# Kernel tuning notes

Hardware: AMD Instinct MI355X
Metric: run time of the kernel (lower is better)

The kernel has to match this reference:

```python
import jax, jax.numpy as jnp
import numpy as np

BS, NQ, D = 4, 12500, 256
HEADS, LEVELS, POINTS = 8, 2, 4
HD = D // HEADS
D_FF = 2048
SHAPES = ((100, 100), (50, 50))   # (H, W) per level; sum(H*W) == NQ
STARTS = (0, 10000)


def layer_norm(x, g, b, eps=1e-5):
    m = x.mean(-1, keepdims=True)
    v = ((x - m) ** 2).mean(-1, keepdims=True)
    return (x - m) * jax.lax.rsqrt(v + eps) * g + b


def bilinear_sample(value_l, loc, H, W):
    # value_l: (bs, heads, H*W, hd); loc: (bs, heads, nq, P, 2) normalized [0,1]
    # matches F.grid_sample(align_corners=False, padding_mode='zeros')
    x = loc[..., 0] * W - 0.5
    y = loc[..., 1] * H - 0.5
    x0 = jnp.floor(x)
    y0 = jnp.floor(y)
    wx1 = x - x0
    wy1 = y - y0
    wx0 = 1.0 - wx1
    wy0 = 1.0 - wy1
    x0i = x0.astype(jnp.int32)
    y0i = y0.astype(jnp.int32)

    def gather(xi, yi):
        valid = (xi >= 0) & (xi < W) & (yi >= 0) & (yi < H)
        idx = jnp.clip(yi, 0, H - 1) * W + jnp.clip(xi, 0, W - 1)  # (bs,heads,nq,P)
        b, h, nq, P = idx.shape
        g = jnp.take_along_axis(value_l, idx.reshape(b, h, nq * P, 1), axis=2)
        g = g.reshape(b, h, nq, P, -1)
        return g * valid[..., None].astype(g.dtype)

    g00 = gather(x0i, y0i)
    g10 = gather(x0i + 1, y0i)
    g01 = gather(x0i, y0i + 1)
    g11 = gather(x0i + 1, y0i + 1)
    return (g00 * (wx0 * wy0)[..., None] + g10 * (wx1 * wy0)[..., None]
            + g01 * (wx0 * wy1)[..., None] + g11 * (wx1 * wy1)[..., None])


def setup_inputs() -> dict:
    key = jax.random.key(0)
    ks = jax.random.split(key, 20)
    s = 0.02
    inp = {
        'query': jax.random.normal(ks[0], (BS, NQ, D), jnp.float32),
        'reference_points': jax.random.uniform(ks[1], (BS, NQ, LEVELS, 2), jnp.float32),
        'w_off': s * jax.random.normal(ks[2], (D, HEADS * LEVELS * POINTS * 2), jnp.float32),
        'b_off': s * jax.random.normal(ks[3], (HEADS * LEVELS * POINTS * 2,), jnp.float32),
        'w_attn': s * jax.random.normal(ks[4], (D, HEADS * LEVELS * POINTS), jnp.float32),
        'b_attn': s * jax.random.normal(ks[5], (HEADS * LEVELS * POINTS,), jnp.float32),
        'w_val': s * jax.random.normal(ks[6], (D, D), jnp.float32),
        'b_val': jnp.zeros((D,), jnp.float32),
        'w_out': s * jax.random.normal(ks[7], (D, D), jnp.float32),
        'b_out': jnp.zeros((D,), jnp.float32),
        'w1': s * jax.random.normal(ks[8], (D, D_FF), jnp.float32),
        'b1': jnp.zeros((D_FF,), jnp.float32),
        'w2': s * jax.random.normal(ks[9], (D_FF, D), jnp.float32),
        'b2': jnp.zeros((D,), jnp.float32),
        'ln0_g': jnp.ones((D,), jnp.float32),
        'ln0_b': jnp.zeros((D,), jnp.float32),
        'ln1_g': jnp.ones((D,), jnp.float32),
        'ln1_b': jnp.zeros((D,), jnp.float32),
    }
    return inp


def reference(query, reference_points, w_off, b_off, w_attn, b_attn, w_val, b_val,
              w_out, b_out, w1, b1, w2, b2, ln0_g, ln0_b, ln1_g, ln1_b):
    bs, nq, _ = query.shape
    # value projection; encoder self-attention: value == query tokens
    value = (query @ w_val + b_val).reshape(bs, nq, HEADS, HD).transpose(0, 2, 1, 3)  # (bs,heads,nv,hd)
    off = (query @ w_off + b_off).reshape(bs, nq, HEADS, LEVELS, POINTS, 2)
    aw = (query @ w_attn + b_attn).reshape(bs, nq, HEADS, LEVELS * POINTS)
    aw = jax.nn.softmax(aw, axis=-1).reshape(bs, nq, HEADS, LEVELS, POINTS)

    out = jnp.zeros((bs, HEADS, nq, HD), query.dtype)
    for l, (H, W) in enumerate(SHAPES):
        normalizer = jnp.array([W, H], query.dtype)
        # (bs,nq,heads,P,2)
        loc = reference_points[:, :, None, l, None, :] + off[:, :, :, l] / normalizer
        loc = loc.transpose(0, 2, 1, 3, 4)  # (bs,heads,nq,P,2)
        v_l = value[:, :, STARTS[l]:STARTS[l] + H * W]  # (bs,heads,H*W,hd)
        sampled = bilinear_sample(v_l, loc, H, W)       # (bs,heads,nq,P,hd)
        w_l = aw[:, :, :, l].transpose(0, 2, 1, 3)      # (bs,heads,nq,P)
        out = out + (sampled * w_l[..., None]).sum(axis=3)

    attn_out = out.transpose(0, 2, 1, 3).reshape(bs, nq, D) @ w_out + b_out
    x = layer_norm(query + attn_out, ln0_g, ln0_b)
    h = jax.nn.relu(x @ w1 + b1)
    x = layer_norm(x + (h @ w2 + b2), ln1_g, ln1_b)
    return x
```

## Files before the change

### kernel.cpp

```cpp
#include <hip/hip_runtime.h>


#define NQv 12500
#define BSv 4
#define Dv  256
#define DFF 2048

typedef __attribute__((ext_vector_type(8))) __bf16 bf16x8;
typedef __attribute__((ext_vector_type(4))) float f32x4;

__device__ __forceinline__ ushort f32_to_bf16(float f) {
  unsigned u = __float_as_uint(f);
  u += 0x7FFFu + ((u >> 16) & 1u);
  return (ushort)(u >> 16);
}
__device__ __forceinline__ float bf16_to_f32(ushort u) {
  return __uint_as_float(((unsigned)u) << 16);
}

__global__ __launch_bounds__(256) void conv_bf16_kernel(
    const float* __restrict__ in, ushort* __restrict__ out, int n4) {
  int i = blockIdx.x * 256 + threadIdx.x;
  if (i >= n4) return;
  float4 v = reinterpret_cast<const float4*>(in)[i];
  uint2 st;
  st.x = (unsigned)f32_to_bf16(v.x) | ((unsigned)f32_to_bf16(v.y) << 16);
  st.y = (unsigned)f32_to_bf16(v.z) | ((unsigned)f32_to_bf16(v.w) << 16);
  reinterpret_cast<uint2*>(out)[i] = st;
}

__global__ __launch_bounds__(256) void ttrans_kernel(
    const float* __restrict__ in, ushort* __restrict__ out, int K, int N) {
  __shared__ ushort tl[64][65];
  const int n0 = blockIdx.x * 64, k0 = blockIdx.y * 64;
  const int t = threadIdx.x;
#pragma unroll
  for (int i = 0; i < 16; ++i) {
    int idx = t + 256 * i;
    int r = idx >> 6, c = idx & 63;
    tl[r][c] = f32_to_bf16(in[(size_t)(k0 + r) * N + n0 + c]);
  }
  __syncthreads();
#pragma unroll
  for (int i = 0; i < 16; ++i) {
    int idx = t + 256 * i;
    int r = idx >> 6, c = idx & 63;
    out[(size_t)(n0 + r) * K + k0 + c] = tl[c][r];
  }
}

__global__ __launch_bounds__(256) void build_wcat_kernel(
    const float* __restrict__ w_val, const float* __restrict__ w_off,
    const float* __restrict__ w_attn, const float* __restrict__ b_val,
    const float* __restrict__ b_off, const float* __restrict__ b_attn,
    ushort* __restrict__ wcat, float* __restrict__ bcat) {
  int i = blockIdx.x * 256 + threadIdx.x;
  if (i < 448 * 256) {
    int n = i >> 8, k = i & 255;
    float v = (n < 256) ? w_val[(size_t)k * 256 + n]
              : (n < 384) ? w_off[(size_t)k * 128 + (n - 256)]
                          : w_attn[(size_t)k * 64 + (n - 384)];
    wcat[i] = f32_to_bf16(v);
  }
  if (i < 512)
    bcat[i] = (i < 256) ? b_val[i] : (i < 384) ? b_off[i - 256]
              : (i < 448) ? b_attn[i - 384] : 0.f;
}

#define TBM 128
#define TBN 128
#define TBK 32

template <int RELU, int NMASK>
__global__ __launch_bounds__(256) void gemm128_kernel(
    const ushort* __restrict__ A, const ushort* __restrict__ Bt,
    const float* __restrict__ bias, ushort* __restrict__ C,
    int M, int K, int ldc, int Nreal) {
  __shared__ ushort lds[4][TBM * TBK];

  const int t = threadIdx.x;
  const int wid = t >> 6, lane = t & 63;
  const int wr = wid >> 1, wc = wid & 1;
  const int m0 = blockIdx.y * TBM;
  const int n0 = blockIdx.x * TBN;

  int srowA[2], srowB[2], gsl[2];
#pragma unroll
  for (int i = 0; i < 2; i++) {
    int row = i * 64 + (t >> 2);
    int ar = m0 + row;
    srowA[i] = (ar < M) ? ar : (M - 1);
    srowB[i] = n0 + row;
    gsl[i] = ((t & 3) ^ ((row >> 1) & 3)) * 8;
  }

  f32x4 acc[4][4] = {};
  const int nt = K / TBK;
  int cur = 0;

#pragma unroll
  for (int i = 0; i < 2; i++) {
    const int ldsoff = (i * 256 + wid * 64) * 8;
    __builtin_amdgcn_global_load_lds(
        (const __attribute__((address_space(1))) void*)(A + (size_t)srowA[i] * K + gsl[i]),
        (__attribute__((address_space(3))) void*)(lds[0] + ldsoff), 16, 0, 0);
    __builtin_amdgcn_global_load_lds(
        (const __attribute__((address_space(1))) void*)(Bt + (size_t)srowB[i] * K + gsl[i]),
        (__attribute__((address_space(3))) void*)(lds[1] + ldsoff), 16, 0, 0);
  }
  __syncthreads();

  const int rl = lane & 15, kh = lane >> 4;
  for (int tk = 0; tk < nt; ++tk) {
    if (tk + 1 < nt) {
      const int k0 = (tk + 1) * TBK;
      const int nb = (cur ^ 1) * 2;
#pragma unroll
      for (int i = 0; i < 2; i++) {
        const int ldsoff = (i * 256 + wid * 64) * 8;
        __builtin_amdgcn_global_load_lds(
            (const __attribute__((address_space(1))) void*)(A + (size_t)srowA[i] * K + k0 + gsl[i]),
            (__attribute__((address_space(3))) void*)(lds[nb] + ldsoff), 16, 0, 0);
        __builtin_amdgcn_global_load_lds(
            (const __attribute__((address_space(1))) void*)(Bt + (size_t)srowB[i] * K + k0 + gsl[i]),
            (__attribute__((address_space(3))) void*)(lds[nb + 1] + ldsoff), 16, 0, 0);
      }
    }
    {
      const ushort* As = lds[cur * 2];
      const ushort* Bs = lds[cur * 2 + 1];
      bf16x8 afr[4], bfr[4];
#pragma unroll
      for (int ni = 0; ni < 4; ni++) {
        int rowb = wc * 64 + ni * 16 + rl;
        int p = kh ^ ((rowb >> 1) & 3);
        bfr[ni] = *reinterpret_cast<const bf16x8*>(Bs + rowb * 32 + p * 8);
      }
#pragma unroll
      for (int mi = 0; mi < 4; mi++) {
        int rowa = wr * 64 + mi * 16 + rl;
        int p = kh ^ ((rowa >> 1) & 3);
        afr[mi] = *reinterpret_cast<const bf16x8*>(As + rowa * 32 + p * 8);
      }
#pragma unroll
      for (int mi = 0; mi < 4; mi++)
#pragma unroll
        for (int ni = 0; ni < 4; ni++)
          acc[mi][ni] = __builtin_amdgcn_mfma_f32_16x16x32_bf16(afr[mi], bfr[ni], acc[mi][ni], 0, 0, 0);
    }
    __syncthreads();
    cur ^= 1;
  }

  ushort* ldsC = lds[0];
  const int rgrp = lane >> 4, cl = lane & 15;
#pragma unroll
  for (int pass = 0; pass < 2; ++pass) {
    if (wr == pass) {
#pragma unroll
      for (int mi = 0; mi < 4; mi++) {
#pragma unroll
        for (int ni = 0; ni < 4; ni++) {
          int col = wc * 64 + ni * 16 + cl;
          float bv = bias[n0 + col];
#pragma unroll
          for (int r = 0; r < 4; r++) {
            int rloc = mi * 16 + rgrp * 4 + r;
            float v = acc[mi][ni][r] + bv;
            if (RELU) v = fmaxf(v, 0.f);
            ldsC[rloc * 132 + col] = f32_to_bf16(v);
          }
        }
      }
    }
    __syncthreads();
    {
      int rloc = t >> 2;
      int row = m0 + pass * 64 + rloc;
      if (row < M) {
#pragma unroll
        for (int j = 0; j < 4; j++) {
          int col = (t & 3) * 32 + j * 8;
          if (!NMASK || n0 + col < Nreal) {
            uint4 v = *reinterpret_cast<const uint4*>(ldsC + rloc * 132 + col);
            *reinterpret_cast<uint4*>(C + (size_t)row * ldc + n0 + col) = v;
          }
        }
      }
    }
    __syncthreads();
  }
}

__global__ __launch_bounds__(512, 1) void ffn_ln_fused_kernel(
    const ushort* __restrict__ xb,
    const ushort* __restrict__ w1t,
    const float* __restrict__ b1,
    const ushort* __restrict__ w2t,
    const float* __restrict__ b2,
    const float* __restrict__ g1, const float* __restrict__ be1,
    float* __restrict__ out,
    int M) {
  __shared__ ushort lds_all[74752];
  ushort* As = lds_all;
  ushort* Hs = lds_all + 32768;
  ushort* stg0 = lds_all + 50176;

  const int t = threadIdx.x;
  const int wv = t >> 6;
  const int wm = wv >> 2;
  const int wn = wv & 3;
  const int lane = t & 63;
  const int rl = lane & 15, kq = lane >> 4;
  const int cl = lane & 15, g4 = lane >> 4;
  const int m0 = blockIdx.x * 128;

  const int b1row = t >> 3, b1slot = t & 7;
  const int b2row = t >> 2, b2slot = t & 3;

  auto stg = [&](int i) { return stg0 + i * 8192; };

  auto issueB1 = [&](int p, int j, ushort* dst) {
#pragma unroll
    for (int ii = 0; ii < 2; ++ii) {
      int row = b1row + 64 * ii;
      int g = b1slot ^ (row & 7);
      __builtin_amdgcn_global_load_lds(
          (const __attribute__((address_space(1))) void*)(
              w1t + (size_t)(p * 128 + row) * 256 + j * 64 + g * 8),
          (__attribute__((address_space(3))) void*)(dst + (t + 512 * ii) * 8), 16, 0, 0);
    }
  };
  auto issueB2 = [&](int p, int tt, ushort* dst) {
#pragma unroll
    for (int ii = 0; ii < 2; ++ii) {
      int row = b2row + 128 * ii;
      int g = b2slot ^ ((row >> 1) & 3);
      __builtin_amdgcn_global_load_lds(
          (const __attribute__((address_space(1))) void*)(
              w2t + (size_t)row * 2048 + p * 128 + tt * 32 + g * 8),
          (__attribute__((address_space(3))) void*)(dst + (t + 512 * ii) * 8), 16, 0, 0);
    }
  };

#pragma unroll
  for (int ii = 0; ii < 8; ++ii) {
    int row = (t >> 5) + 16 * ii;
    int g = (t & 31) ^ (row & 7);
    int ar = m0 + row; ar = (ar < M) ? ar : (M - 1);
    __builtin_amdgcn_global_load_lds(
        (const __attribute__((address_space(1))) void*)(xb + (size_t)ar * 256 + g * 8),
        (__attribute__((address_space(3))) void*)(As + (t + 512 * ii) * 8), 16, 0, 0);
  }
  issueB1(0, 0, stg(0));
  issueB1(0, 1, stg(1));

  f32x4 acc1[4][2] = {};
  f32x4 accF[4][4] = {};
  int cur = 0;

  for (int p = 0; p < 16; ++p) {
#pragma unroll
    for (int j = 0; j < 8; ++j) {
      int tgt = cur + 2; if (tgt >= 3) tgt -= 3;
      if (j <= 5) {
        const int j2 = j + 2;
        const int p2 = p + (j2 >> 3);
        if ((j2 & 7) < 4) issueB1(p2, j2 & 3, stg(tgt));
        else issueB2(p2, (j2 & 7) - 4, stg(tgt));
        asm volatile("s_waitcnt vmcnt(4) lgkmcnt(0)" ::: "memory");
      } else if (p < 15) {
        const int j2m = (j + 2) & 7;
        issueB1(p + 1, j2m, stg(tgt));
        asm volatile("s_waitcnt vmcnt(4) lgkmcnt(0)" ::: "memory");
      } else if (j == 6) {
        asm volatile("s_waitcnt vmcnt(2) lgkmcnt(0)" ::: "memory");
      } else {
        asm volatile("s_waitcnt vmcnt(0) lgkmcnt(0)" ::: "memory");
      }
      __builtin_amdgcn_s_barrier();
      __builtin_amdgcn_sched_barrier(0);

      const ushort* Bs = stg(cur);
      if (j < 4) {
        __builtin_amdgcn_s_setprio(1);
#pragma unroll
        for (int kk = 0; kk < 2; ++kk) {
          bf16x8 afr[4], bfr[2];
          const int slotA = j * 8 + kk * 4 + kq;
#pragma unroll
          for (int mi = 0; mi < 4; mi++) {
            int rowa = wm * 64 + mi * 16 + rl;
            afr[mi] = *reinterpret_cast<const bf16x8*>(As + rowa * 256 + (slotA ^ (rowa & 7)) * 8);
          }
          const int slotB = kk * 4 + kq;
#pragma unroll
          for (int ni = 0; ni < 2; ni++) {
            int rowb = wn * 32 + ni * 16 + rl;
            bfr[ni] = *reinterpret_cast<const bf16x8*>(Bs + rowb * 64 + (slotB ^ (rowb & 7)) * 8);
          }
#pragma unroll
          for (int mi = 0; mi < 4; mi++)
#pragma unroll
            for (int ni = 0; ni < 2; ni++)
              acc1[mi][ni] = __builtin_amdgcn_mfma_f32_16x16x32_bf16(afr[mi], bfr[ni], acc1[mi][ni], 0, 0, 0);
        }
        __builtin_amdgcn_s_setprio(0);
        if (j == 3) {
#pragma unroll
          for (int ni = 0; ni < 2; ni++) {
            int col = wn * 32 + ni * 16 + cl;
            float b1v = b1[p * 128 + col];
#pragma unroll
            for (int mi = 0; mi < 4; mi++) {
#pragma unroll
              for (int r = 0; r < 4; r++) {
                int row = wm * 64 + mi * 16 + g4 * 4 + r;
                Hs[row * 136 + col] = f32_to_bf16(fmaxf(acc1[mi][ni][r] + b1v, 0.f));
              }
            }
          }
#pragma unroll
          for (int mi = 0; mi < 4; mi++)
#pragma unroll
            for (int ni = 0; ni < 2; ni++)
              acc1[mi][ni] = (f32x4){0.f, 0.f, 0.f, 0.f};
        }
      } else {
        const int tt = j - 4;
        bf16x8 afr[4], bfr[4];
#pragma unroll
        for (int mi = 0; mi < 4; mi++) {
          int rowa = wm * 64 + mi * 16 + rl;
          afr[mi] = *reinterpret_cast<const bf16x8*>(Hs + rowa * 136 + (tt * 4 + kq) * 8);
        }
#pragma unroll
        for (int ni = 0; ni < 4; ni++) {
          int rowb = wn * 64 + ni * 16 + rl;
          bfr[ni] = *reinterpret_cast<const bf16x8*>(Bs + rowb * 32 + (kq ^ ((rowb >> 1) & 3)) * 8);
        }
        __builtin_amdgcn_s_setprio(1);
#pragma unroll
        for (int mi = 0; mi < 4; mi++)
#pragma unroll
          for (int ni = 0; ni < 4; ni++)
            accF[mi][ni] = __builtin_amdgcn_mfma_f32_16x16x32_bf16(afr[mi], bfr[ni], accF[mi][ni], 0, 0, 0);
        __builtin_amdgcn_s_setprio(0);
      }
      cur = cur + 1; if (cur >= 3) cur -= 3;
    }
  }

  float* ptab = (float*)stg0;
  float* mtab = (float*)(stg0 + 2048);

  float b2c[4], g1c[4], bec[4];
#pragma unroll
  for (int ni = 0; ni < 4; ni++) {
    int col = wn * 64 + ni * 16 + cl;
    b2c[ni] = b2[col]; g1c[ni] = g1[col]; bec[ni] = be1[col];
  }
#pragma unroll
  for (int mi = 0; mi < 4; mi++) {
#pragma unroll
    for (int ni = 0; ni < 4; ni++) {
      int col = wn * 64 + ni * 16 + cl;
#pragma unroll
      for (int r = 0; r < 4; r++) {
        int row = wm * 64 + mi * 16 + g4 * 4 + r;
        ushort xv = As[row * 256 + ((col >> 3) ^ (row & 7)) * 8 + (col & 7)];
        accF[mi][ni][r] += b2c[ni] + bf16_to_f32(xv);
      }
    }
  }
#pragma unroll
  for (int mi = 0; mi < 4; mi++) {
#pragma unroll
    for (int r = 0; r < 4; r++) {
      float s = accF[mi][0][r] + accF[mi][1][r] + accF[mi][2][r] + accF[mi][3][r];
      float sq = accF[mi][0][r] * accF[mi][0][r] + accF[mi][1][r] * accF[mi][1][r] +
                 accF[mi][2][r] * accF[mi][2][r] + accF[mi][3][r] * accF[mi][3][r];
#pragma unroll
      for (int o = 1; o < 16; o <<= 1) {
        s += __shfl_xor(s, o, 64);
        sq += __shfl_xor(sq, o, 64);
      }
      if (cl == 0) {
        int row = wm * 64 + mi * 16 + g4 * 4 + r;
        ptab[(row * 4 + wn) * 2 + 0] = s;
        ptab[(row * 4 + wn) * 2 + 1] = sq;
      }
    }
  }
  __syncthreads();
  {
    int row = t >> 2, part = t & 3;
    float s = ptab[(row * 4 + part) * 2 + 0];
    float sq = ptab[(row * 4 + part) * 2 + 1];
    s += __shfl_xor(s, 1, 64);  sq += __shfl_xor(sq, 1, 64);
    s += __shfl_xor(s, 2, 64);  sq += __shfl_xor(sq, 2, 64);
    if (part == 0) {
      float mean = s * (1.f / 256.f);
      float var = sq * (1.f / 256.f) - mean * mean;
      mtab[row * 2 + 0] = mean;
      mtab[row * 2 + 1] = rsqrtf(var + 1e-5f);
    }
  }
  __syncthreads();
#pragma unroll
  for (int mi = 0; mi < 4; mi++) {
#pragma unroll
    for (int r = 0; r < 4; r++) {
      int row = wm * 64 + mi * 16 + g4 * 4 + r;
      float2 ms = *reinterpret_cast<const float2*>(mtab + row * 2);
      int grow = m0 + row;
      if (grow < M) {
#pragma unroll
        for (int ni = 0; ni < 4; ni++) {
          int col = wn * 64 + ni * 16 + cl;
          out[(size_t)grow * 256 + col] = (accF[mi][ni][r] - ms.x) * ms.y * g1c[ni] + bec[ni];
        }
      }
    }
  }
}

__global__ __launch_bounds__(256) void deform_attn_kernel(
    const ushort* __restrict__ pcat, const float* __restrict__ refp,
    ushort* __restrict__ out, int total) {
  int tid = blockIdx.x * 256 + threadIdx.x;
  if (tid >= total) return;
  int c0 = (tid & 3) * 8;
  int idx = tid >> 2;
  int h = idx & 7;
  int row = idx >> 3;
  int bl = row / NQv;

  const ushort* prow = pcat + (size_t)row * 448;

  ushort awr[8];
  *reinterpret_cast<uint4*>(awr) = *reinterpret_cast<const uint4*>(prow + 384 + h * 8);
  float lg[8], mx = -1e30f;
#pragma unroll
  for (int i = 0; i < 8; i++) { lg[i] = bf16_to_f32(awr[i]); mx = fmaxf(mx, lg[i]); }
  float ssum = 0.f;
#pragma unroll
  for (int i = 0; i < 8; i++) { lg[i] = __expf(lg[i] - mx); ssum += lg[i]; }
  float inv = 1.f / ssum;

  ushort ofr[16];
  *reinterpret_cast<uint4*>(ofr)     = *reinterpret_cast<const uint4*>(prow + 256 + h * 16);
  *reinterpret_cast<uint4*>(ofr + 8) = *reinterpret_cast<const uint4*>(prow + 256 + h * 16 + 8);
  float4 rp = *reinterpret_cast<const float4*>(refp + (size_t)row * 4);

  float acc8[8] = {};
  const int Ws[2] = {100, 50}, Hs2[2] = {100, 50}, Ss[2] = {0, 10000};
#pragma unroll
  for (int l = 0; l < 2; l++) {
    const int W = Ws[l], H = Hs2[l];
    float fx = (l ? rp.z : rp.x) * (float)W - 0.5f;
    float fy = (l ? rp.w : rp.y) * (float)H - 0.5f;
    const ushort* vbase = pcat + ((size_t)bl * NQv + Ss[l]) * 448 + h * 32 + c0;
#pragma unroll
    for (int p = 0; p < 4; p++) {
      float x = fx + bf16_to_f32(ofr[l * 8 + p * 2 + 0]);
      float y = fy + bf16_to_f32(ofr[l * 8 + p * 2 + 1]);
      float x0f = floorf(x), y0f = floorf(y);
      float wx1 = x - x0f, wy1 = y - y0f;
      float wx0 = 1.f - wx1, wy0 = 1.f - wy1;
      int x0 = (int)x0f, y0 = (int)y0f;
      float aw = lg[l * 4 + p] * inv;

      float cw[4] = {aw * wx0 * wy0, aw * wx1 * wy0, aw * wx0 * wy1, aw * wx1 * wy1};
      int cx[4] = {x0, x0 + 1, x0, x0 + 1};
      int cy[4] = {y0, y0, y0 + 1, y0 + 1};
#pragma unroll
      for (int c = 0; c < 4; c++) {
        int xi = cx[c], yi = cy[c];
        if (xi >= 0 && xi < W && yi >= 0 && yi < H) {
          ushort vr[8];
          *reinterpret_cast<uint4*>(vr) =
              *reinterpret_cast<const uint4*>(vbase + (size_t)(yi * W + xi) * 448);
          float w = cw[c];
#pragma unroll
          for (int j = 0; j < 8; j++) acc8[j] += w * bf16_to_f32(vr[j]);
        }
      }
    }
  }

  ushort st[8];
#pragma unroll
  for (int j = 0; j < 8; j++) st[j] = f32_to_bf16(acc8[j]);
  *reinterpret_cast<uint4*>(out + (size_t)row * 256 + h * 32 + c0) =
      *reinterpret_cast<uint4*>(st);
}

__global__ __launch_bounds__(256) void ln0_kernel(
    const float* __restrict__ A, const ushort* __restrict__ B,
    const float* __restrict__ gamma, const float* __restrict__ beta,
    ushort* __restrict__ outb, int M) {
  int row = blockIdx.x * 4 + (threadIdx.x >> 6);
  int lane = threadIdx.x & 63;
  if (row >= M) return;
  size_t base = (size_t)row * 256 + lane * 4;
  float4 a = *reinterpret_cast<const float4*>(A + base);
  uint2 braw = *reinterpret_cast<const uint2*>(B + base);
  float x0 = a.x + bf16_to_f32((ushort)(braw.x & 0xffffu));
  float x1 = a.y + bf16_to_f32((ushort)(braw.x >> 16));
  float x2 = a.z + bf16_to_f32((ushort)(braw.y & 0xffffu));
  float x3 = a.w + bf16_to_f32((ushort)(braw.y >> 16));
  float s = x0 + x1 + x2 + x3;
  float sq = x0 * x0 + x1 * x1 + x2 * x2 + x3 * x3;
#pragma unroll
  for (int o = 1; o < 64; o <<= 1) {
    s += __shfl_xor(s, o, 64);
    sq += __shfl_xor(sq, o, 64);
  }
  float mean = s * (1.f / 256.f);
  float var = sq * (1.f / 256.f) - mean * mean;
  float rs = rsqrtf(var + 1e-5f);
  float4 gv = *reinterpret_cast<const float4*>(gamma + lane * 4);
  float4 bv = *reinterpret_cast<const float4*>(beta + lane * 4);
  float o0 = (x0 - mean) * rs * gv.x + bv.x;
  float o1 = (x1 - mean) * rs * gv.y + bv.y;
  float o2 = (x2 - mean) * rs * gv.z + bv.z;
  float o3 = (x3 - mean) * rs * gv.w + bv.w;
  uint2 st;
  st.x = (unsigned)f32_to_bf16(o0) | ((unsigned)f32_to_bf16(o1) << 16);
  st.y = (unsigned)f32_to_bf16(o2) | ((unsigned)f32_to_bf16(o3) << 16);
  *reinterpret_cast<uint2*>(outb + base) = st;
}

extern "C" void kernel_launch(void* const* d_in, const int* in_sizes, int n_in,
                              void* d_out, int out_size, void* d_ws, size_t ws_size,
                              hipStream_t stream) {
  const float* query  = (const float*)d_in[0];
  const float* refp   = (const float*)d_in[1];
  const float* w_off  = (const float*)d_in[2];
  const float* b_off  = (const float*)d_in[3];
  const float* w_attn = (const float*)d_in[4];
  const float* b_attn = (const float*)d_in[5];
  const float* w_val  = (const float*)d_in[6];
  const float* b_val  = (const float*)d_in[7];
  const float* w_out  = (const float*)d_in[8];
  const float* b_out  = (const float*)d_in[9];
  const float* w1     = (const float*)d_in[10];
  const float* b1     = (const float*)d_in[11];
  const float* w2     = (const float*)d_in[12];
  const float* b2     = (const float*)d_in[13];
  const float* ln0g   = (const float*)d_in[14];
  const float* ln0b   = (const float*)d_in[15];
  const float* ln1g   = (const float*)d_in[16];
  const float* ln1b   = (const float*)d_in[17];
  float* outp = (float*)d_out;

  char* ws = (char*)d_ws;
  size_t woff = 0;
  auto walloc = [&](size_t bytes) { size_t r = woff; woff += (bytes + 255) & ~(size_t)255; return r; };
  ushort* wcat = (ushort*)(ws + walloc((size_t)512 * 256 * 2));
  float*  bcat = (float*)(ws + walloc(512 * 4));
  ushort* wqt  = (ushort*)(ws + walloc((size_t)256 * 256 * 2));
  ushort* w1t  = (ushort*)(ws + walloc((size_t)DFF * 256 * 2));
  ushort* w2t  = (ushort*)(ws + walloc((size_t)256 * DFF * 2));
  char* arena = ws + woff;
  size_t arena_sz = (ws_size > woff) ? (ws_size - woff) : 0;

  int nb = ((size_t)BSv * NQv * 1920 + (1u << 20) <= arena_sz) ? BSv : 1;
  const int R = nb * NQv;
  ushort* qb   = (ushort*)arena;
  ushort* pcat = (ushort*)(arena + (size_t)R * 512);
  ushort* samp = (ushort*)(arena + (size_t)R * 1408);
  ushort* proj = qb;
  ushort* xb   = samp;

  build_wcat_kernel<<<dim3(448), dim3(256), 0, stream>>>(
      w_val, w_off, w_attn, b_val, b_off, b_attn, wcat, bcat);
  ttrans_kernel<<<dim3(4, 4), dim3(256), 0, stream>>>(w_out, wqt, Dv, Dv);
  ttrans_kernel<<<dim3(DFF / 64, 4), dim3(256), 0, stream>>>(w1, w1t, Dv, DFF);
  ttrans_kernel<<<dim3(4, DFF / 64), dim3(256), 0, stream>>>(w2, w2t, DFF, Dv);

  const int MT = (R + TBM - 1) / TBM;

  for (int c = 0; c < BSv / nb; c++) {
    const int row0 = c * R;
    const float* qrow = query + (size_t)row0 * Dv;

    conv_bf16_kernel<<<dim3((R * 64 + 255) / 256), dim3(256), 0, stream>>>(qrow, qb, R * 64);

    gemm128_kernel<0, 1><<<dim3(4, MT), dim3(256), 0, stream>>>(
        qb, wcat, bcat, pcat, R, Dv, 448, 448);

    deform_attn_kernel<<<dim3((R * 32 + 255) / 256), dim3(256), 0, stream>>>(
        pcat, refp + (size_t)row0 * 4, samp, R * 32);

    gemm128_kernel<0, 0><<<dim3(2, MT), dim3(256), 0, stream>>>(
        samp, wqt, b_out, proj, R, Dv, 256, 256);

    ln0_kernel<<<dim3((R + 3) / 4), dim3(256), 0, stream>>>(qrow, proj, ln0g, ln0b, xb, R);

    ffn_ln_fused_kernel<<<dim3((R + 127) / 128), dim3(512), 0, stream>>>(
        xb, w1t, b1, w2t, b2, ln1g, ln1b, outp + (size_t)row0 * 256, R);
  }
}
```

Before: 338.4 us.

## Restructure FFN pipeline to load LDS fragments before barrier and overlap MFMA

Reorders the fused FFN main loop so each step issues the next global-to-LDS prefetch first, then reads the A/B fragments into registers, and only then barriers and runs the MFMAs. The wait on outstanding loads moves to the end of the step, and a second barrier is added there. The aim is to overlap LDS fragment reads and global prefetch with MFMA work and to relax the vmcnt waits. In exchange each step now has two barriers and holds more fragment registers at once. The ordering between the stage-buffer writes and reads is subtle, so a synchronisation mistake could give wrong results.

Measured after the change: 357.8 us. +5.8%, slower.

```diff
diff --git a/kernel.cpp b/kernel.cpp
--- a/kernel.cpp
+++ b/kernel.cpp
@@ -254,6 +254,8 @@
   }
   issueB1(0, 0, stg(0));
   issueB1(0, 1, stg(1));
+  asm volatile("s_waitcnt vmcnt(2)" ::: "memory");
+  __builtin_amdgcn_s_barrier();
 
   f32x4 acc1[4][2] = {};
   f32x4 accF[4][4] = {};
@@ -263,90 +265,97 @@
 #pragma unroll
     for (int j = 0; j < 8; ++j) {
       int tgt = cur + 2; if (tgt >= 3) tgt -= 3;
-      if (j <= 5) {
-        const int j2 = j + 2;
-        const int p2 = p + (j2 >> 3);
-        if ((j2 & 7) < 4) issueB1(p2, j2 & 3, stg(tgt));
-        else issueB2(p2, (j2 & 7) - 4, stg(tgt));
-        asm volatile("s_waitcnt vmcnt(4) lgkmcnt(0)" ::: "memory");
-      } else if (p < 15) {
-        const int j2m = (j + 2) & 7;
-        issueB1(p + 1, j2m, stg(tgt));
-        asm volatile("s_waitcnt vmcnt(4) lgkmcnt(0)" ::: "memory");
-      } else if (j == 6) {
-        asm volatile("s_waitcnt vmcnt(2) lgkmcnt(0)" ::: "memory");
-      } else {
-        asm volatile("s_waitcnt vmcnt(0) lgkmcnt(0)" ::: "memory");
-      }
-      __builtin_amdgcn_s_barrier();
-      __builtin_amdgcn_sched_barrier(0);
+      if (!(p == 15 && j >= 6)) {
+        const int j2 = (j + 2) & 7;
+        const int p2 = p + ((j + 2) >> 3);
+        if (j2 < 4) issueB1(p2, j2, stg(tgt));
+        else issueB2(p2, j2 - 4, stg(tgt));
+      }
 
       const ushort* Bs = stg(cur);
+      bf16x8 a1[4][2], b1f[2][2];
+      bf16x8 a2[4], b2f[4];
       if (j < 4) {
-        __builtin_amdgcn_s_setprio(1);
 #pragma unroll
         for (int kk = 0; kk < 2; ++kk) {
-          bf16x8 afr[4], bfr[2];
           const int slotA = j * 8 + kk * 4 + kq;
 #pragma unroll
           for (int mi = 0; mi < 4; mi++) {
             int rowa = wm * 64 + mi * 16 + rl;
-            afr[mi] = *reinterpret_cast<const bf16x8*>(As + rowa * 256 + (slotA ^ (rowa & 7)) * 8);
+            a1[mi][kk] = *reinterpret_cast<const bf16x8*>(As + rowa * 256 + (slotA ^ (rowa & 7)) * 8);
           }
           const int slotB = kk * 4 + kq;
 #pragma unroll
           for (int ni = 0; ni < 2; ni++) {
             int rowb = wn * 32 + ni * 16 + rl;
-            bfr[ni] = *reinterpret_cast<const bf16x8*>(Bs + rowb * 64 + (slotB ^ (rowb & 7)) * 8);
+            b1f[ni][kk] = *reinterpret_cast<const bf16x8*>(Bs + rowb * 64 + (slotB ^ (rowb & 7)) * 8);
           }
+        }
+      } else {
+        const int tt = j - 4;
+#pragma unroll
+        for (int mi = 0; mi < 4; mi++) {
+          int rowa = wm * 64 + mi * 16 + rl;
+          a2[mi] = *reinterpret_cast<const bf16x8*>(Hs + rowa * 136 + (tt * 4 + kq) * 8);
+        }
+#pragma unroll
+        for (int ni = 0; ni < 4; ni++) {
+          int rowb = wn * 64 + ni * 16 + rl;
+          b2f[ni] = *reinterpret_cast<const bf16x8*>(Bs + rowb * 32 + (kq ^ ((rowb >> 1) & 3)) * 8);
+        }
+      }
+
+      __builtin_amdgcn_s_barrier();
+      asm volatile("s_waitcnt lgkmcnt(0)" ::: "memory");
+      __builtin_amdgcn_sched_barrier(0);
+
+      __builtin_amdgcn_s_setprio(1);
+      if (j < 4) {
+#pragma unroll
+        for (int kk = 0; kk < 2; ++kk)
 #pragma unroll
           for (int mi = 0; mi < 4; mi++)
 #pragma unroll
             for (int ni = 0; ni < 2; ni++)
-              acc1[mi][ni] = __builtin_amdgcn_mfma_f32_16x16x32_bf16(afr[mi], bfr[ni], acc1[mi][ni], 0, 0, 0);
-        }
-        __builtin_amdgcn_s_setprio(0);
-        if (j == 3) {
-#pragma unroll
-          for (int ni = 0; ni < 2; ni++) {
-            int col = wn * 32 + ni * 16 + cl;
-            float b1v = b1[p * 128 + col];
-#pragma unroll
-            for (int mi = 0; mi < 4; mi++) {
-#pragma unroll
-              for (int r = 0; r < 4; r++) {
-                int row = wm * 64 + mi * 16 + g4 * 4 + r;
-                Hs[row * 136 + col] = f32_to_bf16(fmaxf(acc1[mi][ni][r] + b1v, 0.f));
-              }
+              acc1[mi][ni] = __builtin_amdgcn_mfma_f32_16x16x32_bf16(a1[mi][kk], b1f[ni][kk], acc1[mi][ni], 0, 0, 0);
+      } else {
+#pragma unroll
+        for (int mi = 0; mi < 4; mi++)
+#pragma unroll
+          for (int ni = 0; ni < 4; ni++)
+            accF[mi][ni] = __builtin_amdgcn_mfma_f32_16x16x32_bf16(a2[mi], b2f[ni], accF[mi][ni], 0, 0, 0);
+      }
+      __builtin_amdgcn_s_setprio(0);
+
+      if (j == 3) {
+#pragma unroll
+        for (int ni = 0; ni < 2; ni++) {
+          int col = wn * 32 + ni * 16 + cl;
+          float b1v = b1[p * 128 + col];
+#pragma unroll
+          for (int mi = 0; mi < 4; mi++) {
+#pragma unroll
+            for (int r = 0; r < 4; r++) {
+              int row = wm * 64 + mi * 16 + g4 * 4 + r;
+              Hs[row * 136 + col] = f32_to_bf16(fmaxf(acc1[mi][ni][r] + b1v, 0.f));
             }
           }
-#pragma unroll
-          for (int mi = 0; mi < 4; mi++)
-#pragma unroll
-            for (int ni = 0; ni < 2; ni++)
-              acc1[mi][ni] = (f32x4){0.f, 0.f, 0.f, 0.f};
-        }
+        }
+#pragma unroll
+        for (int mi = 0; mi < 4; mi++)
+#pragma unroll
+          for (int ni = 0; ni < 2; ni++)
+            acc1[mi][ni] = (f32x4){0.f, 0.f, 0.f, 0.f};
+      }
+
+      if (!(p == 15 && j >= 6)) {
+        asm volatile("s_waitcnt vmcnt(2) lgkmcnt(0)" ::: "memory");
+      } else if (j == 6) {
+        asm volatile("s_waitcnt vmcnt(0) lgkmcnt(0)" ::: "memory");
       } else {
-        const int tt = j - 4;
-        bf16x8 afr[4], bfr[4];
-#pragma unroll
-        for (int mi = 0; mi < 4; mi++) {
-          int rowa = wm * 64 + mi * 16 + rl;
-          afr[mi] = *reinterpret_cast<const bf16x8*>(Hs + rowa * 136 + (tt * 4 + kq) * 8);
-        }
-#pragma unroll
-        for (int ni = 0; ni < 4; ni++) {
-          int rowb = wn * 64 + ni * 16 + rl;
-          bfr[ni] = *reinterpret_cast<const bf16x8*>(Bs + rowb * 32 + (kq ^ ((rowb >> 1) & 3)) * 8);
-        }
-        __builtin_amdgcn_s_setprio(1);
-#pragma unroll
-        for (int mi = 0; mi < 4; mi++)
-#pragma unroll
-          for (int ni = 0; ni < 4; ni++)
-            accF[mi][ni] = __builtin_amdgcn_mfma_f32_16x16x32_bf16(afr[mi], bfr[ni], accF[mi][ni], 0, 0, 0);
-        __builtin_amdgcn_s_setprio(0);
-      }
+        asm volatile("s_waitcnt lgkmcnt(0)" ::: "memory");
+      }
+      __builtin_amdgcn_s_barrier();
       cur = cur + 1; if (cur >= 3) cur -= 3;
     }
   }
```

## Fuse output projection GEMM with residual add and LayerNorm0

Applied to the files above, without the earlier changes.

Replaces the separate out-projection GEMM and ln0 kernel with one kernel. It computes a 64x256 tile with MFMA, double-buffers the B tiles, adds bias and the fp32 query residual, and applies LayerNorm in-register before writing bf16. This removes the bf16 proj intermediate round trip and one launch, and keeps the pre-LN sum in fp32. It also adds an initial wait and barrier to the FFN kernel before its main loop. The cost is a narrower M tile and strided scalar query loads in the epilogue.

After: 328.9 us. 1.03x faster.

```diff
diff --git a/kernel.cpp b/kernel.cpp
--- a/kernel.cpp
+++ b/kernel.cpp
@@ -189,6 +189,156 @@
       }
     }
     __syncthreads();
+  }
+}
+
+__global__ __launch_bounds__(256, 2) void outproj_ln0_kernel(
+    const ushort* __restrict__ samp,
+    const ushort* __restrict__ wqt,
+    const float* __restrict__ bias,
+    const float* __restrict__ query,
+    const float* __restrict__ g0, const float* __restrict__ be0,
+    ushort* __restrict__ xb,
+    int M) {
+  __shared__ ushort lds_all[32768];
+  ushort* As = lds_all;
+  ushort* ring0 = lds_all + 16384;
+
+  const int t = threadIdx.x;
+  const int wv = t >> 6;
+  const int lane = t & 63;
+  const int rl = lane & 15, kq = lane >> 4;
+  const int cl = lane & 15, g4 = lane >> 4;
+  const int m0 = blockIdx.x * 64;
+
+  ushort* ring[2] = {ring0, ring0 + 8192};
+
+  auto issueB = [&](int j, ushort* dst) {
+#pragma unroll
+    for (int ii = 0; ii < 4; ++ii) {
+      int row = (t >> 2) + 64 * ii;
+      int g = (t & 3) ^ ((row >> 1) & 3);
+      __builtin_amdgcn_global_load_lds(
+          (const __attribute__((address_space(1))) void*)(
+              wqt + (size_t)row * 256 + j * 32 + g * 8),
+          (__attribute__((address_space(3))) void*)(dst + ((size_t)t + 256 * ii) * 8), 16, 0, 0);
+    }
+  };
+
+#pragma unroll
+  for (int ii = 0; ii < 8; ++ii) {
+    int row = (t >> 5) + 8 * ii;
+    int g = (t & 31) ^ (row & 7);
+    int ar = m0 + row; ar = (ar < M) ? ar : (M - 1);
+    __builtin_amdgcn_global_load_lds(
+        (const __attribute__((address_space(1))) void*)(samp + (size_t)ar * 256 + g * 8),
+        (__attribute__((address_space(3))) void*)(As + ((size_t)t + 256 * ii) * 8), 16, 0, 0);
+  }
+  issueB(0, ring[0]);
+  __syncthreads();
+
+  f32x4 accF[4][4] = {};
+  int cur = 0;
+
+#pragma unroll
+  for (int j = 0; j < 8; ++j) {
+    if (j + 1 < 8) issueB(j + 1, ring[cur ^ 1]);
+    const ushort* Bs = ring[cur];
+    bf16x8 afr[4], bfr[4];
+    const int slotA = j * 4 + kq;
+#pragma unroll
+    for (int mi = 0; mi < 4; mi++) {
+      int rowa = mi * 16 + rl;
+      afr[mi] = *reinterpret_cast<const bf16x8*>(As + rowa * 256 + (slotA ^ (rowa & 7)) * 8);
+    }
+#pragma unroll
+    for (int ni = 0; ni < 4; ni++) {
+      int rowb = wv * 64 + ni * 16 + rl;
+      bfr[ni] = *reinterpret_cast<const bf16x8*>(Bs + rowb * 32 + (kq ^ ((rowb >> 1) & 3)) * 8);
+    }
+    __builtin_amdgcn_s_setprio(1);
+#pragma unroll
+    for (int mi = 0; mi < 4; mi++)
+#pragma unroll
+      for (int ni = 0; ni < 4; ni++)
+        accF[mi][ni] = __builtin_amdgcn_mfma_f32_16x16x32_bf16(afr[mi], bfr[ni], accF[mi][ni], 0, 0, 0);
+    __builtin_amdgcn_s_setprio(0);
+    __syncthreads();
+    cur ^= 1;
+  }
+
+  float* ptab = (float*)ring0;
+  float* mtab = (float*)(ring0 + 2048);
+
+  float bc[4], gc[4], bec[4];
+#pragma unroll
+  for (int ni = 0; ni < 4; ni++) {
+    int col = wv * 64 + ni * 16 + cl;
+    bc[ni] = bias[col]; gc[ni] = g0[col]; bec[ni] = be0[col];
+  }
+#pragma unroll
+  for (int mi = 0; mi < 4; mi++) {
+#pragma unroll
+    for (int ni = 0; ni < 4; ni++) {
+      int col = wv * 64 + ni * 16 + cl;
+#pragma unroll
+      for (int r = 0; r < 4; r++) {
+        int row = mi * 16 + g4 * 4 + r;
+        int qrow = m0 + row; qrow = (qrow < M) ? qrow : (M - 1);
+        accF[mi][ni][r] += bc[ni] + query[(size_t)qrow * 256 + col];
+      }
+    }
+  }
+#pragma unroll
+  for (int mi = 0; mi < 4; mi++) {
+#pragma unroll
+    for (int r = 0; r < 4; r++) {
+      float s = accF[mi][0][r] + accF[mi][1][r] + accF[mi][2][r] + accF[mi][3][r];
+      float sq = accF[mi][0][r] * accF[mi][0][r] + accF[mi][1][r] * accF[mi][1][r] +
+                 accF[mi][2][r] * accF[mi][2][r] + accF[mi][3][r] * accF[mi][3][r];
+#pragma unroll
+      for (int o = 1; o < 16; o <<= 1) {
+        s += __shfl_xor(s, o, 64);
+        sq += __shfl_xor(sq, o, 64);
+      }
+      if (cl == 0) {
+        int row = mi * 16 + g4 * 4 + r;
+        ptab[(row * 4 + wv) * 2 + 0] = s;
+        ptab[(row * 4 + wv) * 2 + 1] = sq;
+      }
+    }
+  }
+  __syncthreads();
+  {
+    int row = t >> 2, part = t & 3;
+    float s = ptab[(row * 4 + part) * 2 + 0];
+    float sq = ptab[(row * 4 + part) * 2 + 1];
+    s += __shfl_xor(s, 1, 64);  sq += __shfl_xor(sq, 1, 64);
+    s += __shfl_xor(s, 2, 64);  sq += __shfl_xor(sq, 2, 64);
+    if (part == 0) {
+      float mean = s * (1.f / 256.f);
+      float var = sq * (1.f / 256.f) - mean * mean;
+      mtab[row * 2 + 0] = mean;
+      mtab[row * 2 + 1] = rsqrtf(var + 1e-5f);
+    }
+  }
+  __syncthreads();
+#pragma unroll
+  for (int mi = 0; mi < 4; mi++) {
+#pragma unroll
+    for (int r = 0; r < 4; r++) {
+      int row = mi * 16 + g4 * 4 + r;
+      float2 ms = *reinterpret_cast<const float2*>(mtab + row * 2);
+      int grow = m0 + row;
+      if (grow < M) {
+#pragma unroll
+        for (int ni = 0; ni < 4; ni++) {
+          int col = wv * 64 + ni * 16 + cl;
+          xb[(size_t)grow * 256 + col] =
+              f32_to_bf16((accF[mi][ni][r] - ms.x) * ms.y * gc[ni] + bec[ni]);
+        }
+      }
+    }
   }
 }
 
@@ -254,6 +404,8 @@
   }
   issueB1(0, 0, stg(0));
   issueB1(0, 1, stg(1));
+  asm volatile("s_waitcnt vmcnt(2)" ::: "memory");
+  __builtin_amdgcn_s_barrier();
 
   f32x4 acc1[4][2] = {};
   f32x4 accF[4][4] = {};
@@ -328,23 +480,23 @@
         }
       } else {
         const int tt = j - 4;
-        bf16x8 afr[4], bfr[4];
+        bf16x8 a2f[4], b2f[4];
 #pragma unroll
         for (int mi = 0; mi < 4; mi++) {
           int rowa = wm * 64 + mi * 16 + rl;
-          afr[mi] = *reinterpret_cast<const bf16x8*>(Hs + rowa * 136 + (tt * 4 + kq) * 8);
+          a2f[mi] = *reinterpret_cast<const bf16x8*>(Hs + rowa * 136 + (tt * 4 + kq) * 8);
         }
 #pragma unroll
         for (int ni = 0; ni < 4; ni++) {
           int rowb = wn * 64 + ni * 16 + rl;
-          bfr[ni] = *reinterpret_cast<const bf16x8*>(Bs + rowb * 32 + (kq ^ ((rowb >> 1) & 3)) * 8);
+          b2f[ni] = *reinterpret_cast<const bf16x8*>(Bs + rowb * 32 + (kq ^ ((rowb >> 1) & 3)) * 8);
         }
         __builtin_amdgcn_s_setprio(1);
 #pragma unroll
         for (int mi = 0; mi < 4; mi++)
 #pragma unroll
           for (int ni = 0; ni < 4; ni++)
-            accF[mi][ni] = __builtin_amdgcn_mfma_f32_16x16x32_bf16(afr[mi], bfr[ni], accF[mi][ni], 0, 0, 0);
+            accF[mi][ni] = __builtin_amdgcn_mfma_f32_16x16x32_bf16(a2f[mi], b2f[ni], accF[mi][ni], 0, 0, 0);
         __builtin_amdgcn_s_setprio(0);
       }
       cur = cur + 1; if (cur >= 3) cur -= 3;
@@ -494,42 +646,6 @@
   for (int j = 0; j < 8; j++) st[j] = f32_to_bf16(acc8[j]);
   *reinterpret_cast<uint4*>(out + (size_t)row * 256 + h * 32 + c0) =
       *reinterpret_cast<uint4*>(st);
-}
-
-__global__ __launch_bounds__(256) void ln0_kernel(
-    const float* __restrict__ A, const ushort* __restrict__ B,
-    const float* __restrict__ gamma, const float* __restrict__ beta,
-    ushort* __restrict__ outb, int M) {
-  int row = blockIdx.x * 4 + (threadIdx.x >> 6);
-  int lane = threadIdx.x & 63;
-  if (row >= M) return;
-  size_t base = (size_t)row * 256 + lane * 4;
-  float4 a = *reinterpret_cast<const float4*>(A + base);
-  uint2 braw = *reinterpret_cast<const uint2*>(B + base);
-  float x0 = a.x + bf16_to_f32((ushort)(braw.x & 0xffffu));
-  float x1 = a.y + bf16_to_f32((ushort)(braw.x >> 16));
-  float x2 = a.z + bf16_to_f32((ushort)(braw.y & 0xffffu));
-  float x3 = a.w + bf16_to_f32((ushort)(braw.y >> 16));
-  float s = x0 + x1 + x2 + x3;
-  float sq = x0 * x0 + x1 * x1 + x2 * x2 + x3 * x3;
-#pragma unroll
-  for (int o = 1; o < 64; o <<= 1) {
-    s += __shfl_xor(s, o, 64);
-    sq += __shfl_xor(sq, o, 64);
-  }
-  float mean = s * (1.f / 256.f);
-  float var = sq * (1.f / 256.f) - mean * mean;
-  float rs = rsqrtf(var + 1e-5f);
-  float4 gv = *reinterpret_cast<const float4*>(gamma + lane * 4);
-  float4 bv = *reinterpret_cast<const float4*>(beta + lane * 4);
-  float o0 = (x0 - mean) * rs * gv.x + bv.x;
-  float o1 = (x1 - mean) * rs * gv.y + bv.y;
-  float o2 = (x2 - mean) * rs * gv.z + bv.z;
-  float o3 = (x3 - mean) * rs * gv.w + bv.w;
-  uint2 st;
-  st.x = (unsigned)f32_to_bf16(o0) | ((unsigned)f32_to_bf16(o1) << 16);
-  st.y = (unsigned)f32_to_bf16(o2) | ((unsigned)f32_to_bf16(o3) << 16);
-  *reinterpret_cast<uint2*>(outb + base) = st;
 }
 
 extern "C" void kernel_launch(void* const* d_in, const int* in_sizes, int n_in,
@@ -571,8 +687,7 @@
   ushort* qb   = (ushort*)arena;
   ushort* pcat = (ushort*)(arena + (size_t)R * 512);
   ushort* samp = (ushort*)(arena + (size_t)R * 1408);
-  ushort* proj = qb;
-  ushort* xb   = samp;
+  ushort* xb   = qb;
 
   build_wcat_kernel<<<dim3(448), dim3(256), 0, stream>>>(
       w_val, w_off, w_attn, b_val, b_off, b_attn, wcat, bcat);
@@ -594,10 +709,8 @@
     deform_attn_kernel<<<dim3((R * 32 + 255) / 256), dim3(256), 0, stream>>>(
         pcat, refp + (size_t)row0 * 4, samp, R * 32);
 
-    gemm128_kernel<0, 0><<<dim3(2, MT), dim3(256), 0, stream>>>(
-        samp, wqt, b_out, proj, R, Dv, 256, 256);
-
-    ln0_kernel<<<dim3((R + 3) / 4), dim3(256), 0, stream>>>(qrow, proj, ln0g, ln0b, xb, R);
+    outproj_ln0_kernel<<<dim3((R + 63) / 64), dim3(256), 0, stream>>>(
+        samp, wqt, b_out, qrow, ln0g, ln0b, xb, R);
 
     ffn_ln_fused_kernel<<<dim3((R + 127) / 128), dim3(512), 0, stream>>>(
         xb, w1t, b1, w2t, b2, ln1g, ln1b, outp + (size_t)row0 * 256, R);
```
